# Kernel tuning notes

Measured on AMD Instinct MI355X. Metric: run time of the kernel, lower is better.

## Reference

```python
import jax, jax.numpy as jnp
import numpy as np

ATOM_FEAT = 128
FILTERS = 128


def setup_inputs() -> dict:
    key = jax.random.key(0)
    k1, k2, k3, k4 = jax.random.split(key, 4)
    B, N, F, C = 8, 128, ATOM_FEAT, 3
    scalar_features = jax.random.normal(k1, (B, N, F), dtype=jnp.float32)
    distances = jax.random.normal(k2, (B, N, N, C), dtype=jnp.float32)
    # xavier_uniform with gain=1.414
    gain = 1.414
    limit_W = gain * np.sqrt(6.0 / (2 * F + FILTERS))
    W = jax.random.uniform(k3, (2 * F, FILTERS), dtype=jnp.float32, minval=-limit_W, maxval=limit_W)
    limit_b = gain * np.sqrt(6.0 / (1 + FILTERS))
    b = jax.random.uniform(k4, (1, FILTERS), dtype=jnp.float32, minval=-limit_b, maxval=limit_b)
    return {"scalar_features": scalar_features, "distances": distances, "W": W, "b": b}


def reference(scalar_features, distances, W, b):
    # scalar_features: [B, N, F]; distances: [B, N, N, C]
    # W: [2F, filters]; b: [1, filters]
    F = scalar_features.shape[-1]
    # Original concatenates repeated features [h_i, h_j] then applies W.
    # Equivalent fused form: split W into halves so the [B,N,N,2F] tensor
    # is never materialized: pair[b,i,j] = h_i @ W1 + h_j @ W2 + b.
    # NOTE: original repeats along dim 2 then transposes(1,2), so the
    # concat at (i,j) is [h_j, h_i] in torch indexing terms; broadcast below
    # matches: s1 broadcast over j-axis, s2 over i-axis per that layout.
    W1, W2 = W[:F], W[F:]
    s_first = jnp.einsum('bnf,fk->bnk', scalar_features, W1)   # [B, N, filters]
    s_second = jnp.einsum('bnf,fk->bnk', scalar_features, W2)  # [B, N, filters]
    # torch: scalar_features (repeated along dim2) varies with i (dim1), constant over j
    pair = s_first[:, :, None, :] + s_second[:, None, :, :] + b  # [B, N, N, filters]
    # vector_features[b,i,j,c,k] = pair[b,i,j,k] * distances[b,i,j,c]
    vector_features = pair[:, :, :, None, :] * distances[..., None]  # [B,N,N,C,filters]
    return vector_features
```

## Files before the change

kernel.cpp:

```cpp
#include <hip/hip_runtime.h>

typedef float v4f __attribute__((ext_vector_type(4)));

#define NATOM 128
#define FEAT 128
#define FILT 128
#define BATCH 8

__global__ __launch_bounds__(256) void s_gemm_kernel(
    const float* __restrict__ sf, const float* __restrict__ W,
    const float* __restrict__ bias, float* __restrict__ s1,
    float* __restrict__ s2) {
  const int row = blockIdx.x;
  const int tid = threadIdx.x;
  const int k = tid & (FILT - 1);
  const int which = tid >> 7;

  __shared__ float sfrow[FEAT];
  if (tid < FEAT) sfrow[tid] = sf[row * FEAT + tid];
  __syncthreads();

  const float* Wcol = W + which * FEAT * FILT + k;
  float acc = 0.f;
#pragma unroll
  for (int f = 0; f < FEAT; ++f) acc = fmaf(sfrow[f], Wcol[f * FILT], acc);

  if (which == 0)
    s1[row * FILT + k] = acc + bias[k];
  else
    s2[row * FILT + k] = acc;
}

__global__ __launch_bounds__(256) void expand_kernel(
    const float* __restrict__ s1, const float* __restrict__ s2,
    const float* __restrict__ dist, float* __restrict__ out) {
  const int blk = blockIdx.x;
  const int bi = blk >> 1;
  const int jh = blk & 1;
  const int b = bi >> 7;
  const int tid = threadIdx.x;
  const int kq = (tid & 31) << 2;
  const int jl = tid >> 5;

  __shared__ float dl[64 * 3];
  const float* dbase = dist + (size_t)bi * NATOM * 3 + jh * 64 * 3;
  if (tid < 192) dl[tid] = dbase[tid];

  const v4f s1v = *reinterpret_cast<const v4f*>(s1 + bi * FILT + kq);
  const float* s2base = s2 + ((size_t)(b << 7) + jh * 64) * FILT;
  float* obase = out + ((size_t)bi * NATOM + jh * 64) * 3 * FILT;

  __syncthreads();

#pragma unroll
  for (int j0 = 0; j0 < 64; j0 += 8) {
    const int jloc = j0 + jl;
    const v4f s2v = *reinterpret_cast<const v4f*>(s2base + jloc * FILT + kq);
    const float d0 = dl[jloc * 3 + 0];
    const float d1 = dl[jloc * 3 + 1];
    const float d2 = dl[jloc * 3 + 2];
    const v4f p = s1v + s2v;
    float* o = obase + (size_t)jloc * 3 * FILT + kq;
    *reinterpret_cast<v4f*>(o) = p * d0;
    *reinterpret_cast<v4f*>(o + FILT) = p * d1;
    *reinterpret_cast<v4f*>(o + 2 * FILT) = p * d2;
  }
}

extern "C" void kernel_launch(void* const* d_in, const int* in_sizes, int n_in,
                              void* d_out, int out_size, void* d_ws, size_t ws_size,
                              hipStream_t stream) {
  const float* sf   = (const float*)d_in[0];
  const float* dist = (const float*)d_in[1];
  const float* W    = (const float*)d_in[2];
  const float* bias = (const float*)d_in[3];
  float* out = (float*)d_out;

  float* s1 = (float*)d_ws;
  float* s2 = s1 + BATCH * NATOM * FILT;

  s_gemm_kernel<<<BATCH * NATOM, 256, 0, stream>>>(sf, W, bias, s1, s2);
  expand_kernel<<<BATCH * NATOM * 2, 256, 0, stream>>>(s1, s2, dist, out);
}
```

Before: 42.76 us.

## Register-block four rows in GEMM and tile expand over i×j blocks

The projection GEMM now computes four output rows per block, so each W load is reused four times from a transposed shared tile, and the grid shrinks by four. The expand kernel now handles a 4×32 (i,j) tile per block, reusing each loaded s2 vector across four i rows. Both changes cut redundant global reads. The expand kernel is bound by the large output write, so the gain may be limited, and the smaller grids (256 and 1024 blocks) lower parallelism.

```diff
diff --git a/kernel.cpp b/kernel.cpp
--- a/kernel.cpp
+++ b/kernel.cpp
@@ -11,59 +11,79 @@
     const float* __restrict__ sf, const float* __restrict__ W,
     const float* __restrict__ bias, float* __restrict__ s1,
     float* __restrict__ s2) {
-  const int row = blockIdx.x;
+  const int r0 = blockIdx.x * 4;
   const int tid = threadIdx.x;
   const int k = tid & (FILT - 1);
   const int which = tid >> 7;
 
-  __shared__ float sfrow[FEAT];
-  if (tid < FEAT) sfrow[tid] = sf[row * FEAT + tid];
+  __shared__ float sfT[FEAT * 4];
+  {
+    const int row = tid >> 7, f0 = tid & 127;
+    sfT[f0 * 4 + row] = sf[(r0 + row) * FEAT + f0];
+    sfT[f0 * 4 + row + 2] = sf[(r0 + row + 2) * FEAT + f0];
+  }
   __syncthreads();
 
   const float* Wcol = W + which * FEAT * FILT + k;
-  float acc = 0.f;
+  v4f acc = {0.f, 0.f, 0.f, 0.f};
 #pragma unroll
-  for (int f = 0; f < FEAT; ++f) acc = fmaf(sfrow[f], Wcol[f * FILT], acc);
+  for (int f = 0; f < FEAT; ++f) {
+    const float w = Wcol[f * FILT];
+    acc += *reinterpret_cast<const v4f*>(&sfT[f * 4]) * w;
+  }
 
-  if (which == 0)
-    s1[row * FILT + k] = acc + bias[k];
-  else
-    s2[row * FILT + k] = acc;
+  float* dst = (which ? s2 : s1) + r0 * FILT + k;
+  const float bb = which ? 0.f : bias[k];
+#pragma unroll
+  for (int r = 0; r < 4; ++r) dst[r * FILT] = acc[r] + bb;
 }
 
 __global__ __launch_bounds__(256) void expand_kernel(
     const float* __restrict__ s1, const float* __restrict__ s2,
     const float* __restrict__ dist, float* __restrict__ out) {
   const int blk = blockIdx.x;
-  const int bi = blk >> 1;
-  const int jh = blk & 1;
-  const int b = bi >> 7;
+  const int jq = blk & 3;
+  const int ig = (blk >> 2) & 31;
+  const int b = blk >> 7;
   const int tid = threadIdx.x;
   const int kq = (tid & 31) << 2;
   const int jl = tid >> 5;
+  const int i0 = ig * 4, j0 = jq * 32;
 
-  __shared__ float dl[64 * 3];
-  const float* dbase = dist + (size_t)bi * NATOM * 3 + jh * 64 * 3;
-  if (tid < 192) dl[tid] = dbase[tid];
+  __shared__ float dl[4 * 32 * 3];
+  {
+    const size_t dbase = ((size_t)(b * NATOM + i0) * NATOM + j0) * 3;
+    for (int idx = tid; idx < 384; idx += 256) {
+      const int ii = idx / 96, rem = idx - ii * 96;
+      dl[idx] = dist[dbase + (size_t)ii * NATOM * 3 + rem];
+    }
+  }
 
-  const v4f s1v = *reinterpret_cast<const v4f*>(s1 + bi * FILT + kq);
-  const float* s2base = s2 + ((size_t)(b << 7) + jh * 64) * FILT;
-  float* obase = out + ((size_t)bi * NATOM + jh * 64) * 3 * FILT;
+  v4f s1v[4];
+#pragma unroll
+  for (int ii = 0; ii < 4; ++ii)
+    s1v[ii] = *reinterpret_cast<const v4f*>(s1 + (b * NATOM + i0 + ii) * FILT + kq);
+
+  const float* s2base = s2 + (size_t)(b * NATOM + j0) * FILT;
+  float* obase0 = out + (((size_t)(b * NATOM + i0) * NATOM + j0) * 3) * FILT;
 
   __syncthreads();
 
 #pragma unroll
-  for (int j0 = 0; j0 < 64; j0 += 8) {
-    const int jloc = j0 + jl;
-    const v4f s2v = *reinterpret_cast<const v4f*>(s2base + jloc * FILT + kq);
-    const float d0 = dl[jloc * 3 + 0];
-    const float d1 = dl[jloc * 3 + 1];
-    const float d2 = dl[jloc * 3 + 2];
-    const v4f p = s1v + s2v;
-    float* o = obase + (size_t)jloc * 3 * FILT + kq;
-    *reinterpret_cast<v4f*>(o) = p * d0;
-    *reinterpret_cast<v4f*>(o + FILT) = p * d1;
-    *reinterpret_cast<v4f*>(o + 2 * FILT) = p * d2;
+  for (int jj0 = 0; jj0 < 32; jj0 += 8) {
+    const int jj = jj0 + jl;
+    const v4f s2v = *reinterpret_cast<const v4f*>(s2base + jj * FILT + kq);
+#pragma unroll
+    for (int ii = 0; ii < 4; ++ii) {
+      const v4f p = s1v[ii] + s2v;
+      const float d0 = dl[(ii * 32 + jj) * 3 + 0];
+      const float d1 = dl[(ii * 32 + jj) * 3 + 1];
+      const float d2 = dl[(ii * 32 + jj) * 3 + 2];
+      float* o = obase0 + (size_t)ii * NATOM * 3 * FILT + (size_t)jj * 3 * FILT + kq;
+      *reinterpret_cast<v4f*>(o) = p * d0;
+      *reinterpret_cast<v4f*>(o + FILT) = p * d1;
+      *reinterpret_cast<v4f*>(o + 2 * FILT) = p * d2;
+    }
   }
 }
 
@@ -79,6 +99,6 @@
   float* s1 = (float*)d_ws;
   float* s2 = s1 + BATCH * NATOM * FILT;
 
-  s_gemm_kernel<<<BATCH * NATOM, 256, 0, stream>>>(sf, W, bias, s1, s2);
-  expand_kernel<<<BATCH * NATOM * 2, 256, 0, stream>>>(s1, s2, dist, out);
+  s_gemm_kernel<<<BATCH * NATOM / 4, 256, 0, stream>>>(sf, W, bias, s1, s2);
+  expand_kernel<<<BATCH * 32 * 4, 256, 0, stream>>>(s1, s2, dist, out);
 }
```

Measured after the change: 66.35 us. 55.2% more time.
